# Kernel optimization log

Measured on AMD Instinct MI355X. Metric: run time of the kernel, lower is better.

The kernel has to match this reference:

```python
import jax, jax.numpy as jnp
import numpy as np

B, C, D, H, W = 2, 2, 160, 192, 224


def setup_inputs() -> dict:
    key = jax.random.key(0)
    k1, k2 = jax.random.split(key)
    I = jax.random.normal(k1, (B, C, D, H, W), dtype=jnp.float32)
    flow = jax.random.normal(k2, (B, 3, D, H, W), dtype=jnp.float32)
    return {"I": I, "flow": flow}


def _warp3d(I, flow):
    # I: [B,C,D,H,W], flow: [B,3,D,H,W] (dx,dy,dz displacements)
    b, c, d, h, w = I.shape
    zz, yy, xx = jnp.meshgrid(
        jnp.arange(d, dtype=jnp.float32),
        jnp.arange(h, dtype=jnp.float32),
        jnp.arange(w, dtype=jnp.float32),
        indexing="ij",
    )
    x = flow[:, 0] + xx  # [B,D,H,W] sample coords
    y = flow[:, 1] + yy
    z = flow[:, 2] + zz

    x0 = jnp.floor(x).astype(jnp.int32)
    y0 = jnp.floor(y).astype(jnp.int32)
    z0 = jnp.floor(z).astype(jnp.int32)
    x1 = jnp.clip(x0 + 1, 0, w - 1)
    y1 = jnp.clip(y0 + 1, 0, h - 1)
    z1 = jnp.clip(z0 + 1, 0, d - 1)
    x0 = jnp.clip(x0, 0, w - 1)
    y0 = jnp.clip(y0, 0, h - 1)
    z0 = jnp.clip(z0, 0, d - 1)

    imf = jnp.transpose(I, (0, 2, 3, 4, 1))  # [B,D,H,W,C]
    bidx = jnp.arange(b)[:, None, None, None]

    def gather(zi, yi, xi):
        return imf[bidx, zi, yi, xi]  # [B,D,H,W,C]

    Ia = gather(z0, y0, x0)
    Ib = gather(z0, y1, x0)
    Ic = gather(z0, y0, x1)
    Id = gather(z0, y1, x1)
    Ie = gather(z1, y0, x0)
    If = gather(z1, y1, x0)
    Ig = gather(z1, y0, x1)
    Ih = gather(z1, y1, x1)

    # Weights use the CLAMPED upper corner, matching the torch source.
    dx = x1.astype(jnp.float32) - x
    dy = y1.astype(jnp.float32) - y
    dz = z1.astype(jnp.float32) - z

    wa = (dz * dx * dy)[..., None]
    wb = (dz * dx * (1 - dy))[..., None]
    wc = (dz * (1 - dx) * dy)[..., None]
    wd = (dz * (1 - dx) * (1 - dy))[..., None]
    we = ((1 - dz) * dx * dy)[..., None]
    wf = ((1 - dz) * dx * (1 - dy))[..., None]
    wg = ((1 - dz) * (1 - dx) * dy)[..., None]
    wh = ((1 - dz) * (1 - dx) * (1 - dy))[..., None]

    out = (wa * Ia + wb * Ib + wc * Ic + wd * Id
           + we * Ie + wf * If + wg * Ig + wh * Ih)  # [B,D,H,W,C]
    return jnp.transpose(out, (0, 4, 1, 2, 3))  # [B,C,D,H,W]


def reference(I, flow):
    return _warp3d(I, flow)
```

## Files before the change

kernel.cpp:

```cpp
#include <hip/hip_runtime.h>

constexpr int B = 2, C = 2, D = 160, H = 192, W = 224;
constexpr int HW = H * W;
constexpr int S  = D * HW;
constexpr int TOTAL = B * S;

__global__ __launch_bounds__(256) void warp3d_kernel(
    const float* __restrict__ I,
    const float* __restrict__ flow,
    float* __restrict__ out)
{
    int idx = blockIdx.x * blockDim.x + threadIdx.x;
    if (idx >= TOTAL) return;

    int b = idx / S;
    int s = idx - b * S;
    int d = s / HW;
    int rem = s - d * HW;
    int h = rem / W;
    int w = rem - h * W;

    const long fb = (long)b * 3 * S + s;
    float fx = flow[fb]         + (float)w;
    float fy = flow[fb + S]     + (float)h;
    float fz = flow[fb + 2 * S] + (float)d;

    int x0 = (int)floorf(fx);
    int y0 = (int)floorf(fy);
    int z0 = (int)floorf(fz);
    int x1 = min(max(x0 + 1, 0), W - 1);
    int y1 = min(max(y0 + 1, 0), H - 1);
    int z1 = min(max(z0 + 1, 0), D - 1);
    x0 = min(max(x0, 0), W - 1);
    y0 = min(max(y0, 0), H - 1);
    z0 = min(max(z0, 0), D - 1);

    float dx = (float)x1 - fx;
    float dy = (float)y1 - fy;
    float dz = (float)z1 - fz;
    float ex = 1.0f - dx, ey = 1.0f - dy, ez = 1.0f - dz;

    float wa = dz * dx * dy;
    float wb = dz * dx * ey;
    float wc = dz * ex * dy;
    float wd = dz * ex * ey;
    float we = ez * dx * dy;
    float wf = ez * dx * ey;
    float wg = ez * ex * dy;
    float wh = ez * ex * ey;

    int oz0 = z0 * HW, oz1 = z1 * HW;
    int oy0 = y0 * W,  oy1 = y1 * W;

    long base = (long)b * C * S;
#pragma unroll
    for (int c = 0; c < C; ++c) {
        const float* __restrict__ Ip = I + base + (long)c * S;
        float va = Ip[oz0 + oy0 + x0];
        float vb = Ip[oz0 + oy1 + x0];
        float vc = Ip[oz0 + oy0 + x1];
        float vd = Ip[oz0 + oy1 + x1];
        float ve = Ip[oz1 + oy0 + x0];
        float vf = Ip[oz1 + oy1 + x0];
        float vg = Ip[oz1 + oy0 + x1];
        float vh = Ip[oz1 + oy1 + x1];
        out[base + (long)c * S + s] =
            wa * va + wb * vb + wc * vc + wd * vd +
            we * ve + wf * vf + wg * vg + wh * vh;
    }
}

extern "C" void kernel_launch(void* const* d_in, const int* in_sizes, int n_in,
                              void* d_out, int out_size, void* d_ws, size_t ws_size,
                              hipStream_t stream) {
    const float* I    = (const float*)d_in[0];
    const float* flow = (const float*)d_in[1];
    float* out = (float*)d_out;

    int block = 256;
    int grid = (TOTAL + block - 1) / block;
    warp3d_kernel<<<grid, block, 0, stream>>>(I, flow, out);
}
```

Measured before the change: 575.5 us.

## Interleave channels into workspace and process two voxels per thread

Adds a pre-pass that rewrites the input from channel-planar to channel-interleaved (float2 per voxel) in the workspace. The warp kernel can then fetch both channels of each corner with one 8-byte gather instead of two separate 4-byte gathers. Each thread now handles two adjacent voxels, using vectorized flow loads and output stores. The cost is an extra full read and write of the input per call, and the new path runs only when the workspace is large enough.

```diff
diff --git a/kernel.cpp b/kernel.cpp
--- a/kernel.cpp
+++ b/kernel.cpp
@@ -5,7 +5,114 @@
 constexpr int S  = D * HW;
 constexpr int TOTAL = B * S;
 
-__global__ __launch_bounds__(256) void warp3d_kernel(
+__global__ __launch_bounds__(256) void interleave_kernel(
+    const float* __restrict__ I, float* __restrict__ ws)
+{
+    long t = (long)blockIdx.x * blockDim.x + threadIdx.x;
+    long s4 = t * 4;
+    if (s4 >= (long)TOTAL) return;
+    int  b = (int)(s4 / S);
+    long s = s4 - (long)b * S;
+
+    const float* Ib = I + (long)b * C * S;
+    float4 a = *(const float4*)(Ib + s);
+    float4 c = *(const float4*)(Ib + S + s);
+
+    float* o = ws + ((long)b * S + s) * 2;
+    *(float4*)(o)     = make_float4(a.x, c.x, a.y, c.y);
+    *(float4*)(o + 4) = make_float4(a.z, c.z, a.w, c.w);
+}
+
+__global__ __launch_bounds__(256, 4) void warp3d_i2(
+    const float2* __restrict__ ws,
+    const float* __restrict__ flow,
+    float* __restrict__ out)
+{
+    constexpr int SP = S / 2;
+    int p = blockIdx.x * blockDim.x + threadIdx.x;
+    if (p >= B * SP) return;
+
+    int b  = p / SP;
+    int sp = p - b * SP;
+    int s  = sp * 2;
+    int d  = s / HW;
+    int rem = s - d * HW;
+    int h  = rem / W;
+    int w  = rem - h * W;
+
+    const float* fl = flow + (long)b * 3 * S;
+    float2 fxv = *(const float2*)(fl + s);
+    float2 fyv = *(const float2*)(fl + S + s);
+    float2 fzv = *(const float2*)(fl + 2 * S + s);
+
+    int   addr[2][8];
+    float wt[2][8];
+#pragma unroll
+    for (int v = 0; v < 2; ++v) {
+        float fx = (v ? fxv.y : fxv.x) + (float)(w + v);
+        float fy = (v ? fyv.y : fyv.x) + (float)h;
+        float fz = (v ? fzv.y : fzv.x) + (float)d;
+
+        int x0 = (int)floorf(fx);
+        int y0 = (int)floorf(fy);
+        int z0 = (int)floorf(fz);
+        int x1 = min(max(x0 + 1, 0), W - 1);
+        int y1 = min(max(y0 + 1, 0), H - 1);
+        int z1 = min(max(z0 + 1, 0), D - 1);
+        x0 = min(max(x0, 0), W - 1);
+        y0 = min(max(y0, 0), H - 1);
+        z0 = min(max(z0, 0), D - 1);
+
+        float dx = (float)x1 - fx;
+        float dy = (float)y1 - fy;
+        float dz = (float)z1 - fz;
+        float ex = 1.0f - dx, ey = 1.0f - dy, ez = 1.0f - dz;
+
+        wt[v][0] = dz * dx * dy;
+        wt[v][1] = dz * dx * ey;
+        wt[v][2] = dz * ex * dy;
+        wt[v][3] = dz * ex * ey;
+        wt[v][4] = ez * dx * dy;
+        wt[v][5] = ez * dx * ey;
+        wt[v][6] = ez * ex * dy;
+        wt[v][7] = ez * ex * ey;
+
+        int z0o = z0 * HW, z1o = z1 * HW;
+        int y0o = y0 * W,  y1o = y1 * W;
+        addr[v][0] = z0o + y0o + x0;
+        addr[v][1] = z0o + y1o + x0;
+        addr[v][2] = z0o + y0o + x1;
+        addr[v][3] = z0o + y1o + x1;
+        addr[v][4] = z1o + y0o + x0;
+        addr[v][5] = z1o + y1o + x0;
+        addr[v][6] = z1o + y0o + x1;
+        addr[v][7] = z1o + y1o + x1;
+    }
+
+    const float2* Ibp = ws + (long)b * S;
+    float2 vals[2][8];
+#pragma unroll
+    for (int v = 0; v < 2; ++v)
+#pragma unroll
+        for (int k = 0; k < 8; ++k)
+            vals[v][k] = Ibp[addr[v][k]];
+
+    float2 o0 = make_float2(0.f, 0.f);
+    float2 o1 = make_float2(0.f, 0.f);
+#pragma unroll
+    for (int k = 0; k < 8; ++k) {
+        o0.x += wt[0][k] * vals[0][k].x;
+        o0.y += wt[0][k] * vals[0][k].y;
+        o1.x += wt[1][k] * vals[1][k].x;
+        o1.y += wt[1][k] * vals[1][k].y;
+    }
+
+    float* ob = out + (long)b * C * S + s;
+    *(float2*)(ob)     = make_float2(o0.x, o1.x);
+    *(float2*)(ob + S) = make_float2(o0.y, o1.y);
+}
+
+__global__ __launch_bounds__(256) void warp3d_direct(
     const float* __restrict__ I,
     const float* __restrict__ flow,
     float* __restrict__ out)
@@ -40,14 +147,8 @@
     float dz = (float)z1 - fz;
     float ex = 1.0f - dx, ey = 1.0f - dy, ez = 1.0f - dz;
 
-    float wa = dz * dx * dy;
-    float wb = dz * dx * ey;
-    float wc = dz * ex * dy;
-    float wd = dz * ex * ey;
-    float we = ez * dx * dy;
-    float wf = ez * dx * ey;
-    float wg = ez * ex * dy;
-    float wh = ez * ex * ey;
+    float wa = dz * dx * dy, wb = dz * dx * ey, wc = dz * ex * dy, wd = dz * ex * ey;
+    float we = ez * dx * dy, wf = ez * dx * ey, wg = ez * ex * dy, wh = ez * ex * ey;
 
     int oz0 = z0 * HW, oz1 = z1 * HW;
     int oy0 = y0 * W,  oy1 = y1 * W;
@@ -77,7 +178,21 @@
     const float* flow = (const float*)d_in[1];
     float* out = (float*)d_out;
 
-    int block = 256;
-    int grid = (TOTAL + block - 1) / block;
-    warp3d_kernel<<<grid, block, 0, stream>>>(I, flow, out);
+    const size_t ws_needed = (size_t)TOTAL * 2 * sizeof(float);
+
+    if (ws_size >= ws_needed) {
+        float* wsf = (float*)d_ws;
+        {
+            int n = TOTAL / 4;
+            interleave_kernel<<<(n + 255) / 256, 256, 0, stream>>>(I, wsf);
+        }
+        {
+            int n = TOTAL / 2;
+            warp3d_i2<<<(n + 255) / 256, 256, 0, stream>>>(
+                (const float2*)wsf, flow, out);
+        }
+    } else {
+        int grid = (TOTAL + 255) / 256;
+        warp3d_direct<<<grid, 256, 0, stream>>>(I, flow, out);
+    }
 }
```

Measured after the change: 549.2 us. 4.6% less time.

## Stage haloed input tiles in LDS for trilinear warp gathers

Applied to the files above, without the earlier changes.

Each block now loads a 3D tile of both input channels into shared memory as float2, with a 4-voxel halo on every side. It then has each thread process 4 depth slices, taking the 8 trilinear corner samples from LDS and falling back to global gathers only when a corner leaves the tile. The aim is to replace scattered global gather traffic with LDS reads, since small random displacements mostly stay inside the halo. The cost is a large halo load of about 7.5x the tile's own volume and roughly 61KB of LDS per block, which limits occupancy. Loading the tile before any compute also serialises each block.

```diff
diff --git a/kernel.cpp b/kernel.cpp
--- a/kernel.cpp
+++ b/kernel.cpp
@@ -3,70 +3,133 @@
 constexpr int B = 2, C = 2, D = 160, H = 192, W = 224;
 constexpr int HW = H * W;
 constexpr int S  = D * HW;
-constexpr int TOTAL = B * S;
 
-__global__ __launch_bounds__(256) void warp3d_kernel(
+constexpr int TD = 4, TH = 8, TW = 32;
+constexpr int M  = 4;
+constexpr int RD = TD + 2 * M;
+constexpr int RH = TH + 2 * M;
+constexpr int RW = TW + 2 * M;
+constexpr int NCELL = RD * RH * RW;
+constexpr int ND = D / TD, NH = H / TH, NW = W / TW;
+constexpr int TILES_PER_B = ND * NH * NW;
+
+__global__ __launch_bounds__(256, 2) void warp3d_tile(
     const float* __restrict__ I,
     const float* __restrict__ flow,
     float* __restrict__ out)
 {
-    int idx = blockIdx.x * blockDim.x + threadIdx.x;
-    if (idx >= TOTAL) return;
+    __shared__ float2 tile[NCELL];
 
-    int b = idx / S;
-    int s = idx - b * S;
-    int d = s / HW;
-    int rem = s - d * HW;
-    int h = rem / W;
-    int w = rem - h * W;
+    int bid = blockIdx.x;
+    int b   = bid / TILES_PER_B;
+    int t   = bid - b * TILES_PER_B;
+    int td  = t / (NH * NW);
+    int r   = t - td * (NH * NW);
+    int th  = r / NW;
+    int tw  = r - th * NW;
+    int d0 = td * TD, h0 = th * TH, w0 = tw * TW;
 
-    const long fb = (long)b * 3 * S + s;
-    float fx = flow[fb]         + (float)w;
-    float fy = flow[fb + S]     + (float)h;
-    float fz = flow[fb + 2 * S] + (float)d;
+    const float* __restrict__ I0 = I + (long)b * 2 * S;
+    const float* __restrict__ I1 = I0 + S;
 
-    int x0 = (int)floorf(fx);
-    int y0 = (int)floorf(fy);
-    int z0 = (int)floorf(fz);
-    int x1 = min(max(x0 + 1, 0), W - 1);
-    int y1 = min(max(y0 + 1, 0), H - 1);
-    int z1 = min(max(z0 + 1, 0), D - 1);
-    x0 = min(max(x0, 0), W - 1);
-    y0 = min(max(y0, 0), H - 1);
-    z0 = min(max(z0, 0), D - 1);
+    for (int c = threadIdx.x; c < NCELL; c += 256) {
+        int rx = c % RW;
+        int t2 = c / RW;
+        int ry = t2 % RH;
+        int rz = t2 / RH;
+        int gz = min(max(d0 - M + rz, 0), D - 1);
+        int gy = min(max(h0 - M + ry, 0), H - 1);
+        int gx = min(max(w0 - M + rx, 0), W - 1);
+        int gi = gz * HW + gy * W + gx;
+        tile[c] = make_float2(I0[gi], I1[gi]);
+    }
+    __syncthreads();
 
-    float dx = (float)x1 - fx;
-    float dy = (float)y1 - fy;
-    float dz = (float)z1 - fz;
-    float ex = 1.0f - dx, ey = 1.0f - dy, ez = 1.0f - dz;
+    int lw = threadIdx.x & 31;
+    int lh = threadIdx.x >> 5;
+    int h = h0 + lh, w = w0 + lw;
+    int base_s = h * W + w;
 
-    float wa = dz * dx * dy;
-    float wb = dz * dx * ey;
-    float wc = dz * ex * dy;
-    float wd = dz * ex * ey;
-    float we = ez * dx * dy;
-    float wf = ez * dx * ey;
-    float wg = ez * ex * dy;
-    float wh = ez * ex * ey;
+    const float* __restrict__ fl = flow + (long)b * 3 * S;
+    float fxr[TD], fyr[TD], fzr[TD];
+#pragma unroll
+    for (int dd = 0; dd < TD; ++dd) {
+        int o = (d0 + dd) * HW + base_s;
+        fxr[dd] = fl[o];
+        fyr[dd] = fl[S + o];
+        fzr[dd] = fl[2 * S + o];
+    }
 
-    int oz0 = z0 * HW, oz1 = z1 * HW;
-    int oy0 = y0 * W,  oy1 = y1 * W;
+    float* __restrict__ ob = out + (long)b * 2 * S;
 
-    long base = (long)b * C * S;
 #pragma unroll
-    for (int c = 0; c < C; ++c) {
-        const float* __restrict__ Ip = I + base + (long)c * S;
-        float va = Ip[oz0 + oy0 + x0];
-        float vb = Ip[oz0 + oy1 + x0];
-        float vc = Ip[oz0 + oy0 + x1];
-        float vd = Ip[oz0 + oy1 + x1];
-        float ve = Ip[oz1 + oy0 + x0];
-        float vf = Ip[oz1 + oy1 + x0];
-        float vg = Ip[oz1 + oy0 + x1];
-        float vh = Ip[oz1 + oy1 + x1];
-        out[base + (long)c * S + s] =
-            wa * va + wb * vb + wc * vc + wd * vd +
-            we * ve + wf * vf + wg * vg + wh * vh;
+    for (int dd = 0; dd < TD; ++dd) {
+        int d = d0 + dd;
+        float X = fxr[dd] + (float)w;
+        float Y = fyr[dd] + (float)h;
+        float Z = fzr[dd] + (float)d;
+
+        int x0 = (int)floorf(X);
+        int y0 = (int)floorf(Y);
+        int z0 = (int)floorf(Z);
+        int x1 = min(max(x0 + 1, 0), W - 1);
+        int y1 = min(max(y0 + 1, 0), H - 1);
+        int z1 = min(max(z0 + 1, 0), D - 1);
+        x0 = min(max(x0, 0), W - 1);
+        y0 = min(max(y0, 0), H - 1);
+        z0 = min(max(z0, 0), D - 1);
+
+        float dx = (float)x1 - X;
+        float dy = (float)y1 - Y;
+        float dz = (float)z1 - Z;
+        float ex = 1.0f - dx, ey = 1.0f - dy, ez = 1.0f - dz;
+
+        float wa = dz * dx * dy, wb = dz * dx * ey;
+        float wc = dz * ex * dy, wdd = dz * ex * ey;
+        float we = ez * dx * dy, wf = ez * dx * ey;
+        float wgg = ez * ex * dy, wh = ez * ex * ey;
+
+        int ix0 = x0 - (w0 - M), ix1 = x1 - (w0 - M);
+        int iy0 = y0 - (h0 - M), iy1 = y1 - (h0 - M);
+        int iz0 = z0 - (d0 - M), iz1 = z1 - (d0 - M);
+
+        bool inr = ((unsigned)ix0 < (unsigned)RW) & ((unsigned)ix1 < (unsigned)RW)
+                 & ((unsigned)iy0 < (unsigned)RH) & ((unsigned)iy1 < (unsigned)RH)
+                 & ((unsigned)iz0 < (unsigned)RD) & ((unsigned)iz1 < (unsigned)RD);
+
+        float2 va, vb, vc, vd, ve, vf, vg, vh;
+        if (inr) {
+            int za = iz0 * (RH * RW), zb = iz1 * (RH * RW);
+            int ya = iy0 * RW,        yb = iy1 * RW;
+            va = tile[za + ya + ix0];
+            vb = tile[za + yb + ix0];
+            vc = tile[za + ya + ix1];
+            vd = tile[za + yb + ix1];
+            ve = tile[zb + ya + ix0];
+            vf = tile[zb + yb + ix0];
+            vg = tile[zb + ya + ix1];
+            vh = tile[zb + yb + ix1];
+        } else {
+            int za = z0 * HW, zb = z1 * HW;
+            int ya = y0 * W,  yb = y1 * W;
+            va = make_float2(I0[za + ya + x0], I1[za + ya + x0]);
+            vb = make_float2(I0[za + yb + x0], I1[za + yb + x0]);
+            vc = make_float2(I0[za + ya + x1], I1[za + ya + x1]);
+            vd = make_float2(I0[za + yb + x1], I1[za + yb + x1]);
+            ve = make_float2(I0[zb + ya + x0], I1[zb + ya + x0]);
+            vf = make_float2(I0[zb + yb + x0], I1[zb + yb + x0]);
+            vg = make_float2(I0[zb + ya + x1], I1[zb + ya + x1]);
+            vh = make_float2(I0[zb + yb + x1], I1[zb + yb + x1]);
+        }
+
+        float o0 = wa * va.x + wb * vb.x + wc * vc.x + wdd * vd.x
+                 + we * ve.x + wf * vf.x + wgg * vg.x + wh * vh.x;
+        float o1 = wa * va.y + wb * vb.y + wc * vc.y + wdd * vd.y
+                 + we * ve.y + wf * vf.y + wgg * vg.y + wh * vh.y;
+
+        int oo = d * HW + base_s;
+        ob[oo]     = o0;
+        ob[S + oo] = o1;
     }
 }
 
@@ -77,7 +140,6 @@
     const float* flow = (const float*)d_in[1];
     float* out = (float*)d_out;
 
-    int block = 256;
-    int grid = (TOTAL + block - 1) / block;
-    warp3d_kernel<<<grid, block, 0, stream>>>(I, flow, out);
+    int grid = B * TILES_PER_B;
+    warp3d_tile<<<grid, 256, 0, stream>>>(I, flow, out);
 }
```

After: 628.8 us. +9.3%, slower.
